# Performance work log

Measured on AMD Instinct MI355X. Metric: run time of the kernel, lower is better.

The kernel has to match this reference:

```python
import jax, jax.numpy as jnp
import numpy as np

LEN_NOISE = 1000
LEN_INTERVAL_U = 50
INPUT_DIM = 3
OUTPUT_DIM = 3
HIDDEN_DIM = 512
LOGSIG_CH = INPUT_DIM + (INPUT_DIM * (INPUT_DIM - 1)) // 2  # depth-2 Lyndon basis: level1 + Levy area


def _static_schedule(window_size):
    """Replicates compute_multilevel_logsignature index logic + the u_logsigrnn
    pop-gating of the forward loop. All quantities are static given window_size."""
    tb = np.linspace(0.0, 1.0, LEN_NOISE)
    tu = tb[::LEN_INTERVAL_U]
    tt = np.linspace(0.0, 1.0, window_size)
    u_indices = np.searchsorted(tb, tu, side='right') - 1
    t_indices = np.searchsorted(tb, tt[1:], side='right') - 1
    u_idx_for_t = np.searchsorted(tu, tt[1:], side='right') - 1
    starts, ends, u_times, last = [], [], [], -1
    for it, iu in zip(t_indices, u_idx_for_t):
        iu = max(int(iu), 0)
        if iu != last:
            u_times.append(float(tu[iu]))
            last = iu
        starts.append(int(u_indices[iu]))
        ends.append(int(it))
    u_times.append(float(tt[-1]))
    gates, q = [], list(u_times)
    for t in tt:  # gate True -> last_h updated to h at this step
        if q and t >= q[0]:
            q.pop(0)
            gates.append(True)
        else:
            gates.append(False)
    return np.array(starts), np.array(ends), np.array(gates)


def _logsig_depth2(path, starts, ends):
    """Depth-2 log-signature (Lyndon basis) of path[:, starts[k]:ends[k]+1] with
    basepoint=True. Level-1 = endpoint (basepoint is 0); level-2 = Levy area,
    computed from a cumulative cross-product prefix sum (basepoint segment
    0 -> path[:,start] contributes zero area)."""
    cross = 0.5 * (path[:, :-1, :, None] * path[:, 1:, None, :]
                   - path[:, :-1, None, :] * path[:, 1:, :, None])  # [B,L-1,d,d]
    C = jnp.cumsum(cross, axis=1)
    C = jnp.concatenate([jnp.zeros_like(C[:, :1]), C], axis=1)      # [B,L,d,d]
    lvl1 = path[:, ends]                                            # [B,T-1,d]
    area = C[:, ends] - C[:, starts]                                # [B,T-1,d,d]
    iu, ju = np.triu_indices(path.shape[-1], k=1)
    return jnp.concatenate([lvl1, area[:, :, iu, ju]], axis=-1)     # [B,T-1,d+C(d,2)]


def setup_inputs() -> dict:
    key = jax.random.key(0)
    ks = jax.random.split(key, 8)
    B, W = 1024, 64
    in_rnn = HIDDEN_DIM + LOGSIG_CH

    def kaiming(k, shape):
        return jax.random.normal(k, shape, jnp.float32) * np.float32(np.sqrt(2.0 / shape[1]))

    return {
        "z": jax.random.normal(ks[0], (B, LEN_NOISE, INPUT_DIM), jnp.float32),
        "W1": kaiming(ks[1], (HIDDEN_DIM, in_rnn)),
        "b1": jnp.zeros((HIDDEN_DIM,), jnp.float32),
        "W2": kaiming(ks[2], (HIDDEN_DIM, HIDDEN_DIM)),
        "b2": jnp.zeros((HIDDEN_DIM,), jnp.float32),
        "W3": kaiming(ks[3], (HIDDEN_DIM, HIDDEN_DIM)),
        "b3": jnp.zeros((HIDDEN_DIM,), jnp.float32),
        "Wout": kaiming(ks[4], (OUTPUT_DIM, HIDDEN_DIM)),
        "batch_size": B,
        "window_size": W,
    }


def reference(z, W1, b1, W2, b2, W3, b3, Wout, batch_size, window_size):
    starts, ends, gates = _static_schedule(window_size)
    # Brownian path: z[:,0]=0, z[:,1:] *= sqrt(dt), cumsum
    dt = 1.0 / (LEN_NOISE - 1)
    zz = z.at[:, 0].set(0.0)
    zz = zz.at[:, 1:].multiply(np.float32(np.sqrt(dt)))
    bp = jnp.cumsum(zz, axis=1)                                     # [B,L,d]
    ls = _logsig_depth2(bp, starts, ends)                           # [B,T-1,ch]
    ls = jnp.concatenate([jnp.zeros_like(ls[:, :1]), ls], axis=1)   # [B,T,ch] (zero prepended)

    def mlp(x):  # FeedForwardNN([h,h]) + Tanh
        h = jax.nn.relu(x @ W1.T + b1)
        h = jax.nn.relu(h @ W2.T + b2)
        return jnp.tanh(h @ W3.T + b3)

    h0 = jnp.zeros((z.shape[0], HIDDEN_DIM), z.dtype)  # init_fixed=True

    def step(last_h, inp):
        ls_t, gate = inp
        h = mlp(jnp.concatenate([last_h, ls_t], axis=-1))
        out = h @ Wout.T  # linear, no bias
        return jnp.where(gate, h, last_h), out

    xs = (jnp.swapaxes(ls, 0, 1), jnp.asarray(gates))
    _, outs = jax.lax.scan(step, h0, xs)                            # [T,B,out]
    return jnp.swapaxes(outs, 0, 1)                                 # [B,T,out]
```

## Files before the change

kernel.cpp:

```cpp
#include <hip/hip_runtime.h>
#include <cmath>

#define WIN 64
#define HID 512
#define BATCH 1024
#define KIN 518

typedef _Float16 f16;
typedef _Float16 half8 __attribute__((ext_vector_type(8)));
typedef float f32x4 __attribute__((ext_vector_type(4)));
typedef unsigned short u16x4 __attribute__((ext_vector_type(4)));

struct Sched { int starts[63]; int ends[63]; };
struct TL { int t[8]; int gf[8]; };
struct Targ { int v[32]; };

__global__ __launch_bounds__(256)
void prep(const float* __restrict__ z, Sched sc, ushort* __restrict__ lsh,
          float scale,
          const float* __restrict__ W1, const float* __restrict__ W2,
          const float* __restrict__ W3, ushort* __restrict__ W1h,
          ushort* __restrict__ W2h, ushort* __restrict__ W3h) {
  const int tid = threadIdx.x;
  if (blockIdx.x >= 1024) {
    const int n1 = HID * (576 / 8);
    const int n2 = HID * (HID / 8);
    int i = (blockIdx.x - 1024) * 256 + tid;
    const float* src; ushort* dst; int Ks, Kd;
    if (i < n1)                 { src = W1; dst = W1h; Ks = KIN; Kd = 576; }
    else if (i < n1 + n2)       { src = W2; dst = W2h; Ks = HID; Kd = HID; i -= n1; }
    else if (i < n1 + 2 * n2)   { src = W3; dst = W3h; Ks = HID; Kd = HID; i -= n1 + n2; }
    else return;
    int nblk = Kd >> 3;
    int row = i / nblk, k = (i - row * nblk) * 8;
    half8 v;
#pragma unroll
    for (int j = 0; j < 8; ++j) {
      int kk = k + j;
      float f = (kk < Ks) ? src[(size_t)row * Ks + kk] : 0.f;
      v[j] = (f16)f;
    }
    *(half8*)&dst[(size_t)row * Kd + k] = v;
    return;
  }
  __shared__ float zs[3000];
  __shared__ float Cs[20][3];
  __shared__ float wtot[4][6];
  __shared__ float earr[63][6];
  __shared__ short fe_s[1000];
  const int b = blockIdx.x;
  const int ln = tid & 63, wv = tid >> 6;

  const float4* zrow = (const float4*)(z + (size_t)b * 3000);
  for (int i = tid; i < 750; i += 256) ((float4*)zs)[i] = zrow[i];
  for (int i = tid; i < 1000; i += 256) fe_s[i] = -1;
  if (tid == 0) { Cs[0][0] = 0.f; Cs[0][1] = 0.f; Cs[0][2] = 0.f; }
  __syncthreads();
  if (tid < 63) fe_s[sc.ends[tid]] = (short)tid;
  __syncthreads();

  const int p0 = 4 * tid + 1;
  int myfe[4];
#pragma unroll
  for (int i = 0; i < 4; ++i) myfe[i] = (p0 + i <= 999) ? fe_s[p0 + i] : -1;

  float d0 = 0.f, d1 = 0.f, d2 = 0.f, A0 = 0.f, A1 = 0.f, A2 = 0.f;
  if (p0 <= 999) {
    float b0 = 0.f, b1 = 0.f, b2 = 0.f;
#pragma unroll
    for (int i = 0; i < 4; ++i) {
      int p = p0 + i;
      if (p > 999) break;
      float n0 = b0 + zs[p * 3 + 0] * scale;
      float n1 = b1 + zs[p * 3 + 1] * scale;
      float n2 = b2 + zs[p * 3 + 2] * scale;
      A0 += 0.5f * (b0 * n1 - b1 * n0);
      A1 += 0.5f * (b0 * n2 - b2 * n0);
      A2 += 0.5f * (b1 * n2 - b2 * n1);
      b0 = n0; b1 = n1; b2 = n2;
    }
    d0 = b0; d1 = b1; d2 = b2;
  }

#pragma unroll
  for (int off = 1; off < 64; off <<= 1) {
    float e0 = __shfl(d0, ln - off), e1 = __shfl(d1, ln - off), e2 = __shfl(d2, ln - off);
    float eA0 = __shfl(A0, ln - off), eA1 = __shfl(A1, ln - off), eA2 = __shfl(A2, ln - off);
    if (ln >= off) {
      A0 = eA0 + A0 + 0.5f * (e0 * d1 - e1 * d0);
      A1 = eA1 + A1 + 0.5f * (e0 * d2 - e2 * d0);
      A2 = eA2 + A2 + 0.5f * (e1 * d2 - e2 * d1);
      d0 += e0; d1 += e1; d2 += e2;
    }
  }
  if (ln == 63) {
    wtot[wv][0] = d0; wtot[wv][1] = d1; wtot[wv][2] = d2;
    wtot[wv][3] = A0; wtot[wv][4] = A1; wtot[wv][5] = A2;
  }
  __syncthreads();

  float P0 = 0.f, P1 = 0.f, P2 = 0.f, PA0 = 0.f, PA1 = 0.f, PA2 = 0.f;
  for (int w = 0; w < wv; ++w) {
    float t0 = wtot[w][0], t1 = wtot[w][1], t2 = wtot[w][2];
    PA0 = PA0 + wtot[w][3] + 0.5f * (P0 * t1 - P1 * t0);
    PA1 = PA1 + wtot[w][4] + 0.5f * (P0 * t2 - P2 * t0);
    PA2 = PA2 + wtot[w][5] + 0.5f * (P1 * t2 - P2 * t1);
    P0 += t0; P1 += t1; P2 += t2;
  }
  float L0 = __shfl(d0, ln - 1), L1 = __shfl(d1, ln - 1), L2 = __shfl(d2, ln - 1);
  float LA0 = __shfl(A0, ln - 1), LA1 = __shfl(A1, ln - 1), LA2 = __shfl(A2, ln - 1);
  if (ln == 0) { L0 = L1 = L2 = LA0 = LA1 = LA2 = 0.f; }
  float bp0 = P0 + L0, bp1 = P1 + L1, bp2 = P2 + L2;
  float C0 = PA0 + LA0 + 0.5f * (P0 * L1 - P1 * L0);
  float C1 = PA1 + LA1 + 0.5f * (P0 * L2 - P2 * L0);
  float C2 = PA2 + LA2 + 0.5f * (P1 * L2 - P2 * L1);

  if (p0 <= 999) {
#pragma unroll
    for (int i = 0; i < 4; ++i) {
      int p = p0 + i;
      if (p > 999) break;
      float n0 = bp0 + zs[p * 3 + 0] * scale;
      float n1 = bp1 + zs[p * 3 + 1] * scale;
      float n2 = bp2 + zs[p * 3 + 2] * scale;
      C0 += 0.5f * (bp0 * n1 - bp1 * n0);
      C1 += 0.5f * (bp0 * n2 - bp2 * n0);
      C2 += 0.5f * (bp1 * n2 - bp2 * n1);
      bp0 = n0; bp1 = n1; bp2 = n2;
      if (p % 50 == 0) {
        int s = p / 50;
        Cs[s][0] = C0; Cs[s][1] = C1; Cs[s][2] = C2;
      }
      int k = myfe[i];
      if (k >= 0) {
        earr[k][0] = bp0; earr[k][1] = bp1; earr[k][2] = bp2;
        earr[k][3] = C0;  earr[k][4] = C1;  earr[k][5] = C2;
      }
    }
  }
  __syncthreads();

  if (tid < 63) {
    int s = sc.starts[tid] / 50;
    half8 v = {};
    v[0] = (f16)earr[tid][0]; v[1] = (f16)earr[tid][1]; v[2] = (f16)earr[tid][2];
    v[3] = (f16)(earr[tid][3] - Cs[s][0]);
    v[4] = (f16)(earr[tid][4] - Cs[s][1]);
    v[5] = (f16)(earr[tid][5] - Cs[s][2]);
    half8 zz = {};
    half8* d = (half8*)(lsh + ((size_t)(tid + 1) * BATCH + b) * 64);
    d[0] = v;
#pragma unroll
    for (int q = 1; q < 8; ++q) d[q] = zz;
  } else if (tid == 63) {
    half8 zz = {};
    half8* d = (half8*)(lsh + (size_t)b * 64);
#pragma unroll
    for (int q = 0; q < 8; ++q) d[q] = zz;
  }
}

template<int FIRST>
__global__ __launch_bounds__(256)
void fused3(const ushort* __restrict__ carry, const ushort* __restrict__ lsh,
            TL tl,
            const ushort* __restrict__ W1h, const ushort* __restrict__ W2h,
            const ushort* __restrict__ W3h,
            const float* __restrict__ b1, const float* __restrict__ b2,
            const float* __restrict__ b3,
            const float* __restrict__ Wout,
            ushort* __restrict__ act1, ushort* __restrict__ act2,
            ushort* __restrict__ Hall, float* __restrict__ outp,
            int* flags, Targ tg) {
  __shared__ ushort lds[32768];
  char* ldsb = (char*)lds;
  const int tid = threadIdx.x;
  const int wv = tid >> 6, ln = tid & 63;
  const int slab = blockIdx.x;
  const int bn0 = blockIdx.y * 128;
  const int slot = slab >> 3;
  const int t = tl.t[slot], gated = tl.gf[slot];
  const int b0 = (slab & 7) * 128;
  const size_t gr0 = (size_t)slab * 128;
  const int xr0 = (wv >> 1) * 64, nr0 = (wv & 1) * 64;
  const int l15 = ln & 15, l4 = ln >> 4;
  const int targ = tg.v[slab];
  const ushort* lbase = lsh + (size_t)t * BATCH * 64;

  f32x4 acc[4][4];

  auto gemm = [&](auto xsrc, const ushort* W, int ldw, int k0, int nk) {
#pragma unroll
    for (int mi = 0; mi < 4; ++mi)
#pragma unroll
      for (int ni = 0; ni < 4; ++ni) acc[mi][ni] = (f32x4){0.f, 0.f, 0.f, 0.f};

    auto stage = [&](int bi, int kt) {
#pragma unroll
      for (int i = 0; i < 4; ++i) {
        int qq = (i * 4 + wv) * 64 + ln;
        int r = qq >> 3, sl = qq & 7, ss = sl ^ (r & 7);
        const ushort* src = xsrc(kt, r, ss);
        __builtin_amdgcn_global_load_lds(
            (const __attribute__((address_space(1))) unsigned int*)src,
            (__attribute__((address_space(3))) unsigned int*)
                (ldsb + bi * 32768 + (i * 4 + wv) * 1024), 16, 0, 0);
      }
#pragma unroll
      for (int i = 0; i < 4; ++i) {
        int qq = (i * 4 + wv) * 64 + ln;
        int r = qq >> 3, sl = qq & 7, ss = sl ^ (r & 7);
        const ushort* src = W + (size_t)(bn0 + r) * ldw + kt * 64 + ss * 8;
        __builtin_amdgcn_global_load_lds(
            (const __attribute__((address_space(1))) unsigned int*)src,
            (__attribute__((address_space(3))) unsigned int*)
                (ldsb + bi * 32768 + 16384 + (i * 4 + wv) * 1024), 16, 0, 0);
      }
    };

    stage(0, k0);
    int cur = 0;
    for (int kt = k0; kt < nk; ++kt) {
      if (kt + 1 < nk) {
        stage(cur ^ 1, kt + 1);
        asm volatile("s_waitcnt vmcnt(8)" ::: "memory");
      } else {
        asm volatile("s_waitcnt vmcnt(0)" ::: "memory");
      }
      __builtin_amdgcn_s_barrier();
      __builtin_amdgcn_sched_barrier(0);
#pragma unroll
      for (int kk = 0; kk < 2; ++kk) {
        half8 xf[4], wf[4];
#pragma unroll
        for (int mi = 0; mi < 4; ++mi) {
          int r = xr0 + mi * 16 + l15;
          int ss = (kk * 4 + l4) ^ (r & 7);
          xf[mi] = *(const half8*)(ldsb + cur * 32768 + r * 128 + ss * 16);
        }
#pragma unroll
        for (int ni = 0; ni < 4; ++ni) {
          int r = nr0 + ni * 16 + l15;
          int ss = (kk * 4 + l4) ^ (r & 7);
          wf[ni] = *(const half8*)(ldsb + cur * 32768 + 16384 + r * 128 + ss * 16);
        }
#pragma unroll
        for (int mi = 0; mi < 4; ++mi)
#pragma unroll
          for (int ni = 0; ni < 4; ++ni)
            acc[mi][ni] = __builtin_amdgcn_mfma_f32_16x16x32_f16(
                wf[ni], xf[mi], acc[mi][ni], 0, 0, 0);
      }
      __builtin_amdgcn_sched_barrier(0);
      asm volatile("s_waitcnt lgkmcnt(0)" ::: "memory");
      __builtin_amdgcn_s_barrier();
      cur ^= 1;
    }
  };

#define EPILOGUE(ACT, BIAS, STORE_STMT)                                       \
  do {                                                                        \
    _Pragma("unroll")                                                         \
    for (int mi = 0; mi < 4; ++mi) {                                          \
      _Pragma("unroll")                                                       \
      for (int ni = 0; ni < 4; ++ni) {                                        \
        int col = bn0 + nr0 + ni * 16 + l4 * 4;                               \
        float4 bv = *(const float4*)&(BIAS)[col];                             \
        float bb[4] = {bv.x, bv.y, bv.z, bv.w};                               \
        union { f16 h[4]; u16x4 u; } cv;                                      \
        _Pragma("unroll")                                                     \
        for (int j4 = 0; j4 < 4; ++j4) {                                      \
          float v = acc[mi][ni][j4] + bb[j4];                                 \
          if (ACT == 1) v = fmaxf(v, 0.f);                                    \
          cv.h[j4] = (f16)v;                                                  \
        }                                                                     \
        STORE_STMT;                                                           \
      }                                                                       \
    }                                                                         \
  } while (0)

#define SYNCSLAB(FI)                                                          \
  do {                                                                        \
    asm volatile("s_waitcnt vmcnt(0)" ::: "memory");                          \
    __syncthreads();                                                          \
    if (tid == 0) {                                                           \
      __hip_atomic_fetch_add(&flags[FI], 1, __ATOMIC_RELAXED,                 \
                             __HIP_MEMORY_SCOPE_AGENT);                       \
      while (__hip_atomic_load(&flags[FI], __ATOMIC_RELAXED,                  \
                               __HIP_MEMORY_SCOPE_AGENT) < targ)              \
        __builtin_amdgcn_s_sleep(2);                                          \
    }                                                                         \
    __syncthreads();                                                          \
  } while (0)

  if (FIRST) {
    gemm([&](int kt, int r, int ss) {
      (void)kt; return lbase + (size_t)(b0 + r) * 64 + ss * 8;
    }, W1h, 576, 8, 9);
  } else {
    gemm([&](int kt, int r, int ss) {
      int b_ = b0 + r;
      return (kt < 8) ? carry + (size_t)b_ * HID + kt * 64 + ss * 8
                      : lbase + (size_t)b_ * 64 + ss * 8;
    }, W1h, 576, 0, 9);
  }
  EPILOGUE(1, b1,
    *(u16x4*)&act1[(gr0 + xr0 + mi * 16 + l15) * 512 + col] = cv.u);
  SYNCSLAB(slab);

  gemm([&](int kt, int r, int ss) {
    return act1 + (gr0 + r) * (size_t)HID + kt * 64 + ss * 8;
  }, W2h, 512, 0, 8);
  EPILOGUE(1, b2,
    *(u16x4*)&act2[(gr0 + xr0 + mi * 16 + l15) * 512 + col] = cv.u);
  SYNCSLAB(64 + slab);

  gemm([&](int kt, int r, int ss) {
    return act2 + (gr0 + r) * (size_t)HID + kt * 64 + ss * 8;
  }, W3h, 512, 0, 8);
  {
    float po[4][3];
#pragma unroll
    for (int mi = 0; mi < 4; ++mi) { po[mi][0] = 0.f; po[mi][1] = 0.f; po[mi][2] = 0.f; }
#pragma unroll
    for (int mi = 0; mi < 4; ++mi) {
#pragma unroll
      for (int ni = 0; ni < 4; ++ni) {
        int col = bn0 + nr0 + ni * 16 + l4 * 4;
        float4 bv = *(const float4*)&b3[col];
        float4 w0 = *(const float4*)&Wout[col];
        float4 w1 = *(const float4*)&Wout[512 + col];
        float4 w2 = *(const float4*)&Wout[1024 + col];
        float bb[4] = {bv.x, bv.y, bv.z, bv.w};
        float W0[4] = {w0.x, w0.y, w0.z, w0.w};
        float W1a[4] = {w1.x, w1.y, w1.z, w1.w};
        float W2a[4] = {w2.x, w2.y, w2.z, w2.w};
        union { f16 h[4]; u16x4 u; } cv;
#pragma unroll
        for (int j4 = 0; j4 < 4; ++j4) {
          float v = acc[mi][ni][j4] + bb[j4];
          float xc = fminf(fmaxf(v, -9.f), 9.f);
          float e = __expf(2.f * xc); v = (e - 1.f) / (e + 1.f);
          cv.h[j4] = (f16)v;
          po[mi][0] += v * W0[j4];
          po[mi][1] += v * W1a[j4];
          po[mi][2] += v * W2a[j4];
        }
        if (gated) {
          size_t hrow = (size_t)t * BATCH + b0 + xr0 + mi * 16 + l15;
          *(u16x4*)&Hall[hrow * 512 + col] = cv.u;
        }
      }
    }
#pragma unroll
    for (int mi = 0; mi < 4; ++mi) {
#pragma unroll
      for (int o = 0; o < 3; ++o) {
        float s = po[mi][o];
        s += __shfl_xor(s, 16);
        s += __shfl_xor(s, 32);
        po[mi][o] = s;
      }
      if (l4 == 0) {
        int row = b0 + xr0 + mi * 16 + l15;
        int y2 = blockIdx.y * 2 + (wv & 1);
        float* op = outp + (((size_t)y2 * WIN + t) * BATCH + row) * 3;
        op[0] = po[mi][0]; op[1] = po[mi][1]; op[2] = po[mi][2];
      }
    }
  }
#undef EPILOGUE
#undef SYNCSLAB
}

__global__ __launch_bounds__(256)
void out_sum(const float* __restrict__ outp, float* __restrict__ out) {
  int idx = blockIdx.x * 256 + threadIdx.x;
  if (idx >= BATCH * WIN * 3) return;
  int o = idx % 3, bt = idx / 3;
  int t = bt % WIN, b = bt / WIN;
  float s = 0.f;
#pragma unroll
  for (int y = 0; y < 8; ++y)
    s += outp[(((size_t)y * WIN + t) * BATCH + b) * 3 + o];
  out[idx] = s;
}

extern "C" void kernel_launch(void* const* d_in, const int* in_sizes, int n_in,
                              void* d_out, int out_size, void* d_ws, size_t ws_size,
                              hipStream_t stream) {
  (void)n_in; (void)out_size; (void)ws_size; (void)in_sizes;
  const float* z    = (const float*)d_in[0];
  const float* W1   = (const float*)d_in[1];
  const float* b1   = (const float*)d_in[2];
  const float* W2   = (const float*)d_in[3];
  const float* b2   = (const float*)d_in[4];
  const float* W3   = (const float*)d_in[5];
  const float* b3   = (const float*)d_in[6];
  const float* Wout = (const float*)d_in[7];
  float* out = (float*)d_out;

  double tb[1000], tt[64], tu[20];
  {
    double sb = 1.0 / 999.0; for (int i = 0; i < 1000; ++i) tb[i] = i * sb; tb[999] = 1.0;
    double st = 1.0 / 63.0;  for (int k = 0; k < 64; ++k)  tt[k] = k * st;  tt[63] = 1.0;
    for (int j = 0; j < 20; ++j) tu[j] = tb[50 * j];
  }
  auto ssr = [](const double* a, int n, double v) -> int {
    int lo = 0, hi = n;
    while (lo < hi) { int mid = (lo + hi) >> 1; if (a[mid] <= v) lo = mid + 1; else hi = mid; }
    return lo - 1;
  };
  Sched sc; int gates[64];
  {
    int u_indices[20];
    for (int j = 0; j < 20; ++j) u_indices[j] = ssr(tb, 1000, tu[j]);
    double u_times[80]; int nut = 0; int last = -1;
    for (int k = 1; k < 64; ++k) {
      int it = ssr(tb, 1000, tt[k]);
      int iu = ssr(tu, 20, tt[k]); if (iu < 0) iu = 0;
      if (iu != last) { u_times[nut++] = tu[iu]; last = iu; }
      sc.starts[k - 1] = u_indices[iu];
      sc.ends[k - 1] = it;
    }
    u_times[nut++] = tt[63];
    int qh = 0;
    for (int k = 0; k < 64; ++k) {
      if (qh < nut && tt[k] >= u_times[qh]) { ++qh; gates[k] = 1; } else gates[k] = 0;
    }
  }
  int seg[64], g[64], ng = 0, jlast = -1;
  for (int t = 0; t < WIN; ++t) {
    seg[t] = jlast;
    if (gates[t]) { g[ng] = t; jlast = ng; ++ng; }
  }

  char* p = (char*)d_ws;
  int* flags   = (int*)p;    p += 128 * 4;
  ushort* lsh  = (ushort*)p; p += (size_t)WIN * BATCH * 64 * 2;
  ushort* W1h  = (ushort*)p; p += (size_t)HID * 576 * 2;
  ushort* W2h  = (ushort*)p; p += (size_t)HID * HID * 2;
  ushort* W3h  = (ushort*)p; p += (size_t)HID * HID * 2;
  ushort* Hall = (ushort*)p; p += (size_t)WIN * BATCH * HID * 2;
  ushort* act1 = (ushort*)p; p += (size_t)4 * BATCH * HID * 2;
  ushort* act2 = (ushort*)p; p += (size_t)4 * BATCH * HID * 2;
  float* outp  = (float*)p;  p += (size_t)8 * WIN * BATCH * 3 * 4;

  hipMemsetAsync(flags, 0, 128 * 4, stream);

  float scale = (float)std::sqrt(1.0 / 999.0);
  prep<<<1024 + 400, 256, 0, stream>>>(z, sc, lsh, scale,
                                       W1, W2, W3, W1h, W2h, W3h);

  Targ tg; for (int i = 0; i < 32; ++i) tg.v[i] = 0;
  for (int r = 0; r < ng; ++r) {
    TL tlr; int cnt = 0;
    for (int t = 0; t < WIN && cnt < 4; ++t)
      if (seg[t] == r - 1) tlr.t[cnt++] = t;
    if (cnt == 0) continue;
    for (int i = cnt; i < 8; ++i) tlr.t[i] = tlr.t[0];
    for (int i = 0; i < 8; ++i) tlr.gf[i] = (tlr.t[i] == g[r]) ? 1 : 0;
    for (int s = 0; s < cnt * 8; ++s) tg.v[s] += 4;
    const ushort* carry = (r == 0) ? nullptr : Hall + (size_t)g[r - 1] * (BATCH * HID);
    dim3 gg(cnt * 8, 4), gb(256);
    if (r == 0)
      fused3<1><<<gg, gb, 0, stream>>>(carry, lsh, tlr, W1h, W2h, W3h,
                                       b1, b2, b3, Wout, act1, act2, Hall,
                                       outp, flags, tg);
    else
      fused3<0><<<gg, gb, 0, stream>>>(carry, lsh, tlr, W1h, W2h, W3h,
                                       b1, b2, b3, Wout, act1, act2, Hall,
                                       outp, flags, tg);
  }

  out_sum<<<(BATCH * WIN * 3 + 255) / 256, 256, 0, stream>>>(outp, out);
}
```

Measured before the change: 614.5 us.

## Replace per-round kernel launches with one persistent kernel using device-side barriers

The series of fused3 launches, one per gated round, is replaced by a single persistent chain_k kernel on a 32x4 grid that loops over rounds. Rounds are separated by a spin barrier keyed on each block's XCD group (slab & 7). The act1/act2 buffers are double-buffered by round parity so a fast group can start the next round without overwriting data still being read. This removes per-launch overhead and the kernel-boundary drain between rounds, at the cost of spin-waiting, a grid that must stay co-resident, and idle blocks in rounds that use fewer than 4 slots.

```diff
diff --git a/kernel.cpp b/kernel.cpp
--- a/kernel.cpp
+++ b/kernel.cpp
@@ -12,8 +12,7 @@
 typedef unsigned short u16x4 __attribute__((ext_vector_type(4)));
 
 struct Sched { int starts[63]; int ends[63]; };
-struct TL { int t[8]; int gf[8]; };
-struct Targ { int v[32]; };
+struct Plan { int ng; int cnt[24]; int g[24]; int tl[24][4]; };
 
 __global__ __launch_bounds__(256)
 void prep(const float* __restrict__ z, Sched sc, ushort* __restrict__ lsh,
@@ -160,18 +159,16 @@
   }
 }
 
-template<int FIRST>
-__global__ __launch_bounds__(256)
-void fused3(const ushort* __restrict__ carry, const ushort* __restrict__ lsh,
-            TL tl,
-            const ushort* __restrict__ W1h, const ushort* __restrict__ W2h,
-            const ushort* __restrict__ W3h,
-            const float* __restrict__ b1, const float* __restrict__ b2,
-            const float* __restrict__ b3,
-            const float* __restrict__ Wout,
-            ushort* __restrict__ act1, ushort* __restrict__ act2,
-            ushort* __restrict__ Hall, float* __restrict__ outp,
-            int* flags, Targ tg) {
+__global__ __launch_bounds__(256, 1)
+void chain_k(const ushort* __restrict__ lsh,
+             const ushort* __restrict__ W1h, const ushort* __restrict__ W2h,
+             const ushort* __restrict__ W3h,
+             const float* __restrict__ b1, const float* __restrict__ b2,
+             const float* __restrict__ b3, const float* __restrict__ Wout,
+             ushort* __restrict__ act1a, ushort* __restrict__ act1b,
+             ushort* __restrict__ act2a, ushort* __restrict__ act2b,
+             ushort* __restrict__ Hall, float* __restrict__ outp,
+             int* flags, Plan pl) {
   __shared__ ushort lds[32768];
   char* ldsb = (char*)lds;
   const int tid = threadIdx.x;
@@ -179,13 +176,12 @@
   const int slab = blockIdx.x;
   const int bn0 = blockIdx.y * 128;
   const int slot = slab >> 3;
-  const int t = tl.t[slot], gated = tl.gf[slot];
   const int b0 = (slab & 7) * 128;
   const size_t gr0 = (size_t)slab * 128;
+  const int xcd = slab & 7;
   const int xr0 = (wv >> 1) * 64, nr0 = (wv & 1) * 64;
   const int l15 = ln & 15, l4 = ln >> 4;
-  const int targ = tg.v[slab];
-  const ushort* lbase = lsh + (size_t)t * BATCH * 64;
+  int lbar = 0;
 
   f32x4 acc[4][4];
 
@@ -258,7 +254,7 @@
     }
   };
 
-#define EPILOGUE(ACT, BIAS, STORE_STMT)                                       \
+#define EPILOGUE_RELU(BIAS, DST)                                              \
   do {                                                                        \
     _Pragma("unroll")                                                         \
     for (int mi = 0; mi < 4; ++mi) {                                          \
@@ -271,105 +267,126 @@
         _Pragma("unroll")                                                     \
         for (int j4 = 0; j4 < 4; ++j4) {                                      \
           float v = acc[mi][ni][j4] + bb[j4];                                 \
-          if (ACT == 1) v = fmaxf(v, 0.f);                                    \
+          v = fmaxf(v, 0.f);                                                  \
           cv.h[j4] = (f16)v;                                                  \
         }                                                                     \
-        STORE_STMT;                                                           \
+        *(u16x4*)&(DST)[(gr0 + xr0 + mi * 16 + l15) * 512 + col] = cv.u;      \
       }                                                                       \
     }                                                                         \
   } while (0)
 
-#define SYNCSLAB(FI)                                                          \
+#define SYNCSLAB()                                                            \
   do {                                                                        \
+    ++lbar;                                                                   \
     asm volatile("s_waitcnt vmcnt(0)" ::: "memory");                          \
     __syncthreads();                                                          \
     if (tid == 0) {                                                           \
-      __hip_atomic_fetch_add(&flags[FI], 1, __ATOMIC_RELAXED,                 \
+      __hip_atomic_fetch_add(&flags[slab], 1, __ATOMIC_RELAXED,               \
                              __HIP_MEMORY_SCOPE_AGENT);                       \
-      while (__hip_atomic_load(&flags[FI], __ATOMIC_RELAXED,                  \
-                               __HIP_MEMORY_SCOPE_AGENT) < targ)              \
+      while (__hip_atomic_load(&flags[slab], __ATOMIC_RELAXED,                \
+                               __HIP_MEMORY_SCOPE_AGENT) < 4 * lbar)          \
         __builtin_amdgcn_s_sleep(2);                                          \
     }                                                                         \
     __syncthreads();                                                          \
   } while (0)
 
-  if (FIRST) {
-    gemm([&](int kt, int r, int ss) {
-      (void)kt; return lbase + (size_t)(b0 + r) * 64 + ss * 8;
-    }, W1h, 576, 8, 9);
-  } else {
-    gemm([&](int kt, int r, int ss) {
-      int b_ = b0 + r;
-      return (kt < 8) ? carry + (size_t)b_ * HID + kt * 64 + ss * 8
-                      : lbase + (size_t)b_ * 64 + ss * 8;
-    }, W1h, 576, 0, 9);
-  }
-  EPILOGUE(1, b1,
-    *(u16x4*)&act1[(gr0 + xr0 + mi * 16 + l15) * 512 + col] = cv.u);
-  SYNCSLAB(slab);
-
-  gemm([&](int kt, int r, int ss) {
-    return act1 + (gr0 + r) * (size_t)HID + kt * 64 + ss * 8;
-  }, W2h, 512, 0, 8);
-  EPILOGUE(1, b2,
-    *(u16x4*)&act2[(gr0 + xr0 + mi * 16 + l15) * 512 + col] = cv.u);
-  SYNCSLAB(64 + slab);
-
-  gemm([&](int kt, int r, int ss) {
-    return act2 + (gr0 + r) * (size_t)HID + kt * 64 + ss * 8;
-  }, W3h, 512, 0, 8);
-  {
-    float po[4][3];
-#pragma unroll
-    for (int mi = 0; mi < 4; ++mi) { po[mi][0] = 0.f; po[mi][1] = 0.f; po[mi][2] = 0.f; }
-#pragma unroll
-    for (int mi = 0; mi < 4; ++mi) {
-#pragma unroll
-      for (int ni = 0; ni < 4; ++ni) {
-        int col = bn0 + nr0 + ni * 16 + l4 * 4;
-        float4 bv = *(const float4*)&b3[col];
-        float4 w0 = *(const float4*)&Wout[col];
-        float4 w1 = *(const float4*)&Wout[512 + col];
-        float4 w2 = *(const float4*)&Wout[1024 + col];
-        float bb[4] = {bv.x, bv.y, bv.z, bv.w};
-        float W0[4] = {w0.x, w0.y, w0.z, w0.w};
-        float W1a[4] = {w1.x, w1.y, w1.z, w1.w};
-        float W2a[4] = {w2.x, w2.y, w2.z, w2.w};
-        union { f16 h[4]; u16x4 u; } cv;
-#pragma unroll
-        for (int j4 = 0; j4 < 4; ++j4) {
-          float v = acc[mi][ni][j4] + bb[j4];
-          float xc = fminf(fmaxf(v, -9.f), 9.f);
-          float e = __expf(2.f * xc); v = (e - 1.f) / (e + 1.f);
-          cv.h[j4] = (f16)v;
-          po[mi][0] += v * W0[j4];
-          po[mi][1] += v * W1a[j4];
-          po[mi][2] += v * W2a[j4];
+  for (int r = 0; r < pl.ng; ++r) {
+    const bool active = (slot < pl.cnt[r]);
+    if (active) {
+      const int t = pl.tl[r][slot];
+      const int gated = (t == pl.g[r]) ? 1 : 0;
+      const ushort* lbase = lsh + (size_t)t * BATCH * 64;
+      ushort* a1 = (r & 1) ? act1b : act1a;
+      ushort* a2 = (r & 1) ? act2b : act2a;
+
+      if (r == 0) {
+        gemm([&](int kt, int rr, int ss) {
+          (void)kt; return lbase + (size_t)(b0 + rr) * 64 + ss * 8;
+        }, W1h, 576, 8, 9);
+      } else {
+        const ushort* carry = Hall + (size_t)pl.g[r - 1] * (BATCH * HID);
+        gemm([&](int kt, int rr, int ss) {
+          int b_ = b0 + rr;
+          return (kt < 8) ? carry + (size_t)b_ * HID + kt * 64 + ss * 8
+                          : lbase + (size_t)b_ * 64 + ss * 8;
+        }, W1h, 576, 0, 9);
+      }
+      EPILOGUE_RELU(b1, a1);
+      SYNCSLAB();
+
+      gemm([&](int kt, int rr, int ss) {
+        return a1 + (gr0 + rr) * (size_t)HID + kt * 64 + ss * 8;
+      }, W2h, 512, 0, 8);
+      EPILOGUE_RELU(b2, a2);
+      SYNCSLAB();
+
+      gemm([&](int kt, int rr, int ss) {
+        return a2 + (gr0 + rr) * (size_t)HID + kt * 64 + ss * 8;
+      }, W3h, 512, 0, 8);
+      {
+        float po[4][3];
+#pragma unroll
+        for (int mi = 0; mi < 4; ++mi) { po[mi][0] = 0.f; po[mi][1] = 0.f; po[mi][2] = 0.f; }
+#pragma unroll
+        for (int mi = 0; mi < 4; ++mi) {
+#pragma unroll
+          for (int ni = 0; ni < 4; ++ni) {
+            int col = bn0 + nr0 + ni * 16 + l4 * 4;
+            float4 bv = *(const float4*)&b3[col];
+            float4 w0 = *(const float4*)&Wout[col];
+            float4 w1 = *(const float4*)&Wout[512 + col];
+            float4 w2 = *(const float4*)&Wout[1024 + col];
+            float bb[4] = {bv.x, bv.y, bv.z, bv.w};
+            float W0[4] = {w0.x, w0.y, w0.z, w0.w};
+            float W1a[4] = {w1.x, w1.y, w1.z, w1.w};
+            float W2a[4] = {w2.x, w2.y, w2.z, w2.w};
+            union { f16 h[4]; u16x4 u; } cv;
+#pragma unroll
+            for (int j4 = 0; j4 < 4; ++j4) {
+              float v = acc[mi][ni][j4] + bb[j4];
+              float xc = fminf(fmaxf(v, -9.f), 9.f);
+              float e = __expf(2.f * xc); v = (e - 1.f) / (e + 1.f);
+              cv.h[j4] = (f16)v;
+              po[mi][0] += v * W0[j4];
+              po[mi][1] += v * W1a[j4];
+              po[mi][2] += v * W2a[j4];
+            }
+            if (gated) {
+              size_t hrow = (size_t)t * BATCH + b0 + xr0 + mi * 16 + l15;
+              *(u16x4*)&Hall[hrow * 512 + col] = cv.u;
+            }
+          }
         }
-        if (gated) {
-          size_t hrow = (size_t)t * BATCH + b0 + xr0 + mi * 16 + l15;
-          *(u16x4*)&Hall[hrow * 512 + col] = cv.u;
+#pragma unroll
+        for (int mi = 0; mi < 4; ++mi) {
+#pragma unroll
+          for (int o = 0; o < 3; ++o) {
+            float s = po[mi][o];
+            s += __shfl_xor(s, 16);
+            s += __shfl_xor(s, 32);
+            po[mi][o] = s;
+          }
+          if (l4 == 0) {
+            int row = b0 + xr0 + mi * 16 + l15;
+            int y2 = blockIdx.y * 2 + (wv & 1);
+            float* op = outp + (((size_t)y2 * WIN + t) * BATCH + row) * 3;
+            op[0] = po[mi][0]; op[1] = po[mi][1]; op[2] = po[mi][2];
+          }
         }
       }
     }
-#pragma unroll
-    for (int mi = 0; mi < 4; ++mi) {
-#pragma unroll
-      for (int o = 0; o < 3; ++o) {
-        float s = po[mi][o];
-        s += __shfl_xor(s, 16);
-        s += __shfl_xor(s, 32);
-        po[mi][o] = s;
-      }
-      if (l4 == 0) {
-        int row = b0 + xr0 + mi * 16 + l15;
-        int y2 = blockIdx.y * 2 + (wv & 1);
-        float* op = outp + (((size_t)y2 * WIN + t) * BATCH + row) * 3;
-        op[0] = po[mi][0]; op[1] = po[mi][1]; op[2] = po[mi][2];
-      }
-    }
-  }
-#undef EPILOGUE
+    asm volatile("s_waitcnt vmcnt(0)" ::: "memory");
+    __syncthreads();
+    if (tid == 0) {
+      __hip_atomic_fetch_add(&flags[32 + xcd], 1, __ATOMIC_RELAXED,
+                             __HIP_MEMORY_SCOPE_AGENT);
+      while (__hip_atomic_load(&flags[32 + xcd], __ATOMIC_RELAXED,
+                               __HIP_MEMORY_SCOPE_AGENT) < 16 * (r + 1))
+        __builtin_amdgcn_s_sleep(2);
+    }
+    __syncthreads();
+  }
+#undef EPILOGUE_RELU
 #undef SYNCSLAB
 }
 
@@ -435,43 +452,39 @@
     if (gates[t]) { g[ng] = t; jlast = ng; ++ng; }
   }
 
+  Plan pl; pl.ng = ng;
+  for (int r = 0; r < ng && r < 24; ++r) {
+    int cnt = 0;
+    for (int t = 0; t < WIN && cnt < 4; ++t)
+      if (seg[t] == r - 1) pl.tl[r][cnt++] = t;
+    pl.cnt[r] = cnt;
+    pl.g[r] = g[r];
+    for (int i = cnt; i < 4; ++i) pl.tl[r][i] = 0;
+  }
+
   char* p = (char*)d_ws;
-  int* flags   = (int*)p;    p += 128 * 4;
-  ushort* lsh  = (ushort*)p; p += (size_t)WIN * BATCH * 64 * 2;
-  ushort* W1h  = (ushort*)p; p += (size_t)HID * 576 * 2;
-  ushort* W2h  = (ushort*)p; p += (size_t)HID * HID * 2;
-  ushort* W3h  = (ushort*)p; p += (size_t)HID * HID * 2;
-  ushort* Hall = (ushort*)p; p += (size_t)WIN * BATCH * HID * 2;
-  ushort* act1 = (ushort*)p; p += (size_t)4 * BATCH * HID * 2;
-  ushort* act2 = (ushort*)p; p += (size_t)4 * BATCH * HID * 2;
-  float* outp  = (float*)p;  p += (size_t)8 * WIN * BATCH * 3 * 4;
-
-  hipMemsetAsync(flags, 0, 128 * 4, stream);
+  int* flags    = (int*)p;    p += 64 * 4;
+  ushort* lsh   = (ushort*)p; p += (size_t)WIN * BATCH * 64 * 2;
+  ushort* W1h   = (ushort*)p; p += (size_t)HID * 576 * 2;
+  ushort* W2h   = (ushort*)p; p += (size_t)HID * HID * 2;
+  ushort* W3h   = (ushort*)p; p += (size_t)HID * HID * 2;
+  ushort* Hall  = (ushort*)p; p += (size_t)WIN * BATCH * HID * 2;
+  ushort* act1a = (ushort*)p; p += (size_t)4 * BATCH * HID * 2;
+  ushort* act1b = (ushort*)p; p += (size_t)4 * BATCH * HID * 2;
+  ushort* act2a = (ushort*)p; p += (size_t)4 * BATCH * HID * 2;
+  ushort* act2b = (ushort*)p; p += (size_t)4 * BATCH * HID * 2;
+  float* outp   = (float*)p;  p += (size_t)8 * WIN * BATCH * 3 * 4;
+
+  hipMemsetAsync(flags, 0, 64 * 4, stream);
 
   float scale = (float)std::sqrt(1.0 / 999.0);
   prep<<<1024 + 400, 256, 0, stream>>>(z, sc, lsh, scale,
                                        W1, W2, W3, W1h, W2h, W3h);
 
-  Targ tg; for (int i = 0; i < 32; ++i) tg.v[i] = 0;
-  for (int r = 0; r < ng; ++r) {
-    TL tlr; int cnt = 0;
-    for (int t = 0; t < WIN && cnt < 4; ++t)
-      if (seg[t] == r - 1) tlr.t[cnt++] = t;
-    if (cnt == 0) continue;
-    for (int i = cnt; i < 8; ++i) tlr.t[i] = tlr.t[0];
-    for (int i = 0; i < 8; ++i) tlr.gf[i] = (tlr.t[i] == g[r]) ? 1 : 0;
-    for (int s = 0; s < cnt * 8; ++s) tg.v[s] += 4;
-    const ushort* carry = (r == 0) ? nullptr : Hall + (size_t)g[r - 1] * (BATCH * HID);
-    dim3 gg(cnt * 8, 4), gb(256);
-    if (r == 0)
-      fused3<1><<<gg, gb, 0, stream>>>(carry, lsh, tlr, W1h, W2h, W3h,
-                                       b1, b2, b3, Wout, act1, act2, Hall,
-                                       outp, flags, tg);
-    else
-      fused3<0><<<gg, gb, 0, stream>>>(carry, lsh, tlr, W1h, W2h, W3h,
-                                       b1, b2, b3, Wout, act1, act2, Hall,
-                                       outp, flags, tg);
-  }
+  chain_k<<<dim3(32, 4), 256, 0, stream>>>(lsh, W1h, W2h, W3h,
+                                           b1, b2, b3, Wout,
+                                           act1a, act1b, act2a, act2b,
+                                           Hall, outp, flags, pl);
 
   out_sum<<<(BATCH * WIN * 3 + 255) / 256, 256, 0, stream>>>(outp, out);
 }
```

After: 640.6 us. 4.2% more time.
